# Optimization experiments

Measured on AMD Instinct MI355X. Metric: run time of the kernel, lower is better.

The kernel has to match this reference:

```python
import jax, jax.numpy as jnp
import numpy as np
import math

B, D, NH, HD, FF, P, IMG = 4, 768, 12, 64, 3072, 16, 256
L = (IMG // P) ** 2      # 256 tokens
PD = P * P * 3           # 768 patch dim
GRID = IMG // P          # 16


def setup_inputs() -> dict:
    key = jax.random.key(0)
    ks = iter(jax.random.split(key, 80))
    def nrm(shape, s=0.02):
        return jax.random.normal(next(ks), shape, jnp.float32) * s
    return {
        "x": jax.random.normal(next(ks), (B, 3, IMG, IMG), jnp.float32),
        "pe_norm_w": jnp.ones((PD,), jnp.float32),
        "pe_proj_w": nrm((PD, D)),
        "pe_proj_b": jnp.zeros((D,), jnp.float32),
        "pe_norm_out_w": jnp.ones((D,), jnp.float32),
        "pos_embed": nrm((1, L, D)),
        "in_attn_norm_w": jnp.ones((6, D), jnp.float32),
        "in_qkv_w": nrm((6, D, 3 * D)),
        "in_out_w": nrm((6, D, D)),
        "in_ff_norm_w": jnp.ones((6, D), jnp.float32),
        "in_w1": nrm((6, D, 2 * FF)),
        "in_w2": nrm((6, FF, D)),
        "mid_attn_norm_w": jnp.ones((3, D), jnp.float32),
        "mid_qkv_w": nrm((3, D, 3 * D)),
        "mid_out_w": nrm((3, D, D)),
        "mid_ff_norm_w": jnp.ones((3, D), jnp.float32),
        "mid_w1": nrm((3, D, 2 * FF)),
        "mid_w2": nrm((3, FF, D)),
        "out_skip_w": nrm((2 * D, D)),
        "out_skip_b": jnp.zeros((D,), jnp.float32),
        "out_attn_norm_w": jnp.ones((D,), jnp.float32),
        "out_qkv_w": nrm((D, 3 * D)),
        "out_out_w": nrm((D, D)),
        "out_ff_norm_w": jnp.ones((D,), jnp.float32),
        "out_w1": nrm((D, 2 * FF)),
        "out_w2": nrm((FF, D)),
        "final_norm_w": jnp.ones((D,), jnp.float32),
        "ol_proj_w": nrm((D, PD)),
        "ol_proj_b": jnp.zeros((PD,), jnp.float32),
        "rb_conv_in_w": nrm((128, 3, 3, 3), 0.1),
        "rb_gn_w": jnp.ones((5, 128), jnp.float32),
        "rb_gn_b": jnp.zeros((5, 128), jnp.float32),
        "rb_conv1_w": nrm((128, 1, 5, 5), 0.1),
        "rb_conv2_w": nrm((128, 1, 5, 5), 0.1),
        "head_conv_w": nrm((1, 128, 3, 3), 0.1),
    }


def _mish(x):
    return x * jnp.tanh(jax.nn.softplus(x))


def _rms(x, w, eps=1e-5):
    return x * jax.lax.rsqrt(jnp.mean(x * x, axis=-1, keepdims=True) + eps) * w


def _attn(x, qkv_w, out_w):
    b, l, _ = x.shape
    q, k, v = jnp.split(x @ qkv_w, 3, axis=-1)
    s = 1.0 / math.sqrt(HD)  # applied to BOTH q and k, as in source
    q = (q * s).reshape(b, l, NH, HD)
    k = (k * s).reshape(b, l, NH, HD)
    v = v.reshape(b, l, NH, HD)
    logits = jnp.einsum('bqhd,bkhd->bhqk', q, k).astype(jnp.float32)
    w = jax.nn.softmax(logits, axis=-1).astype(x.dtype)
    o = jnp.einsum('bhqk,bkhd->bqhd', w, v).reshape(b, l, NH * HD)
    return o @ out_w


def _ff(x, w1, w2):
    a, g = jnp.split(x @ w1, 2, axis=-1)
    return (_mish(a) * g) @ w2


def _block(x, an, qkv, ow, fn, w1, w2):
    x = x + _attn(_rms(x, an), qkv, ow)
    x = x + _ff(_rms(x, fn), w1, w2)
    return x


def _gn(x, w, b, groups=8, eps=1e-5):
    bb, c, h, ww = x.shape
    xg = x.reshape(bb, groups, c // groups, h, ww)
    m = jnp.mean(xg, axis=(2, 3, 4), keepdims=True)
    v = jnp.var(xg, axis=(2, 3, 4), keepdims=True)
    xn = ((xg - m) * jax.lax.rsqrt(v + eps)).reshape(bb, c, h, ww)
    return xn * w[:, None, None] + b[:, None, None]


def _conv(x, w, pad, dil=1, groups=1):
    xp = jnp.pad(x, ((0, 0), (0, 0), (pad, pad), (pad, pad)), mode='reflect')
    return jax.lax.conv_general_dilated(
        xp, w, window_strides=(1, 1), padding='VALID', rhs_dilation=(dil, dil),
        feature_group_count=groups, dimension_numbers=('NCHW', 'OIHW', 'NCHW'))


def _forward(x, pe_norm_w, pe_proj_w, pe_proj_b, pe_norm_out_w, pos_embed,
             in_attn_norm_w, in_qkv_w, in_out_w, in_ff_norm_w, in_w1, in_w2,
             mid_attn_norm_w, mid_qkv_w, mid_out_w, mid_ff_norm_w, mid_w1, mid_w2,
             out_skip_w, out_skip_b, out_attn_norm_w, out_qkv_w, out_out_w,
             out_ff_norm_w, out_w1, out_w2, final_norm_w, ol_proj_w, ol_proj_b,
             rb_conv_in_w, rb_gn_w, rb_gn_b, rb_conv1_w, rb_conv2_w, head_conv_w):
    b = x.shape[0]
    # PatchEmbed: b c (h p1) (w p2) -> b (h w) (p1 p2 c)
    t = x.reshape(b, 3, GRID, P, GRID, P).transpose(0, 2, 4, 3, 5, 1).reshape(b, L, PD)
    t = _rms(t, pe_norm_w)
    t = t @ pe_proj_w + pe_proj_b
    t = _rms(t, pe_norm_out_w)
    t = t + pos_embed
    # U-ViT trunk: 6 in blocks (skips saved), 3 middle, 1 out block (source typo -> single out block)
    skips = []
    for i in range(6):
        t = _block(t, in_attn_norm_w[i], in_qkv_w[i], in_out_w[i],
                   in_ff_norm_w[i], in_w1[i], in_w2[i])
        skips.append(t)
    for i in range(3):
        t = _block(t, mid_attn_norm_w[i], mid_qkv_w[i], mid_out_w[i],
                   mid_ff_norm_w[i], mid_w1[i], mid_w2[i])
    t = jnp.concatenate([t, skips[-1]], axis=-1) @ out_skip_w + out_skip_b
    t = _block(t, out_attn_norm_w, out_qkv_w, out_out_w, out_ff_norm_w, out_w1, out_w2)
    t = _rms(t, final_norm_w)
    # OutBlock: proj, dropout(eval=identity), unpatchify to b 3 256 256
    t = t @ ol_proj_w + ol_proj_b
    img = t.reshape(b, GRID, GRID, P, P, 3).transpose(0, 5, 1, 3, 2, 4).reshape(b, 3, IMG, IMG)
    # ResNetBlock(128)
    h = _conv(img, rb_conv_in_w, 1)
    h = _mish(_gn(h, rb_gn_w[0], rb_gn_b[0]))
    res = h
    h = _mish(_gn(_conv(h, rb_conv1_w, 2, 1, 128), rb_gn_w[1], rb_gn_b[1]))
    h = res + h
    h = _mish(_gn(h, rb_gn_w[2], rb_gn_b[2]))
    res = h
    h = _mish(_gn(_conv(h, rb_conv2_w, 6, 3, 128), rb_gn_w[3], rb_gn_b[3]))
    h = res + h
    h = _mish(_gn(h, rb_gn_w[4], rb_gn_b[4]))
    return _conv(h, head_conv_w, 1)  # [B, 1, 256, 256]


def reference(x, pe_norm_w, pe_proj_w, pe_proj_b, pe_norm_out_w, pos_embed,
              in_attn_norm_w, in_qkv_w, in_out_w, in_ff_norm_w, in_w1, in_w2,
              mid_attn_norm_w, mid_qkv_w, mid_out_w, mid_ff_norm_w, mid_w1, mid_w2,
              out_skip_w, out_skip_b, out_attn_norm_w, out_qkv_w, out_out_w,
              out_ff_norm_w, out_w1, out_w2, final_norm_w, ol_proj_w, ol_proj_b,
              rb_conv_in_w, rb_gn_w, rb_gn_b, rb_conv1_w, rb_conv2_w, head_conv_w):
    return _forward(x, pe_norm_w, pe_proj_w, pe_proj_b, pe_norm_out_w, pos_embed,
                    in_attn_norm_w, in_qkv_w, in_out_w, in_ff_norm_w, in_w1, in_w2,
                    mid_attn_norm_w, mid_qkv_w, mid_out_w, mid_ff_norm_w, mid_w1, mid_w2,
                    out_skip_w, out_skip_b, out_attn_norm_w, out_qkv_w, out_out_w,
                    out_ff_norm_w, out_w1, out_w2, final_norm_w, ol_proj_w, ol_proj_b,
                    rb_conv_in_w, rb_gn_w, rb_gn_b, rb_conv1_w, rb_conv2_w, head_conv_w)
```

## Files before the change

kernel.cpp:

```cpp
#include <hip/hip_runtime.h>
#include <math.h>

#define B_ 4
#define D_ 768
#define NH_ 12
#define HD_ 64
#define FF_ 3072
#define L_ 256
#define PD_ 768
#define GRID_ 16
#define P_ 16
#define IMG_ 256
#define M_ (B_*L_)
#define NCONV_ (B_*128*IMG_*IMG_)

typedef __attribute__((ext_vector_type(8))) short short8;
typedef __attribute__((ext_vector_type(4))) float f32x4;
typedef __attribute__((ext_vector_type(4))) unsigned short us4;
typedef __attribute__((ext_vector_type(8))) unsigned short us8;
typedef unsigned short ushort_t;

__device__ __forceinline__ float mishf(float x){
    float e = __expf(x);
    float u = (1.f + e) * (1.f + e);
    return x * (1.f - 2.f / (u + 1.f));
}

__device__ __forceinline__ int refl(int i, int n){
    if (i < 0) i = -i;
    if (i >= n) i = 2*n - 2 - i;
    return i;
}

__device__ __forceinline__ ushort_t f2bf(float f){
    unsigned int u = __float_as_uint(f);
    unsigned int r = (u + 0x7FFFu + ((u >> 16) & 1u)) >> 16;
    return (ushort_t)r;
}
__device__ __forceinline__ float bf2f(ushort_t u){
    return __uint_as_float(((unsigned int)u) << 16);
}

__device__ __forceinline__ void block_red2(float& s, float& q){
    #pragma unroll
    for (int o = 32; o > 0; o >>= 1){ s += __shfl_down(s, o); q += __shfl_down(q, o); }
    __shared__ float r1[4], r2[4];
    int tid = threadIdx.x;
    if ((tid & 63) == 0){ r1[tid>>6] = s; r2[tid>>6] = q; }
    __syncthreads();
    if (tid == 0){ s = r1[0]+r1[1]+r1[2]+r1[3]; q = r2[0]+r2[1]+r2[2]+r2[3]; }
    __syncthreads();
}

__global__ __launch_bounds__(256) void k_patchify(const float* __restrict__ x, float* __restrict__ t){
    int idx = blockIdx.x*256 + threadIdx.x;
    int d = idx % PD_; int l = (idx/PD_) % L_; int b = idx/(PD_*L_);
    int c = d % 3; int p = d / 3; int p1 = p / P_; int p2 = p % P_;
    int gh = l / GRID_; int gw = l % GRID_;
    int sy = gh*P_ + p1, sx = gw*P_ + p2;
    t[idx] = x[(((size_t)b*3 + c)*IMG_ + sy)*IMG_ + sx];
}

__global__ __launch_bounds__(256) void k_wt(const float* __restrict__ b0, const float* __restrict__ b1,
                                            const float* __restrict__ b2, int n0, int n1,
                                            ushort_t* __restrict__ dst, int K, int N){
    int z = blockIdx.z;
    size_t sz = (size_t)K * N;
    const float* src = (z < n0) ? b0 + (size_t)z*sz
                     : (z < n0+n1) ? b1 + (size_t)(z-n0)*sz
                     : b2 + (size_t)(z-n0-n1)*sz;
    ushort_t* out = dst + (size_t)z*sz;
    __shared__ float ld[32][33];
    int k0 = blockIdx.y*32, nc0 = blockIdx.x*32;
    int tid = threadIdx.x;
    int c = tid & 31, r8 = tid >> 5;
    #pragma unroll
    for (int i = 0; i < 4; ++i){
        int k = r8 + i*8;
        ld[k][c] = src[(size_t)(k0+k)*N + nc0 + c];
    }
    __syncthreads();
    #pragma unroll
    for (int i = 0; i < 4; ++i){
        int n = r8 + i*8;
        out[(size_t)(nc0+n)*K + k0 + c] = f2bf(ld[c][n]);
    }
}

template<bool OUT_BF>
__global__ __launch_bounds__(256) void k_rms(const float* __restrict__ x, const float* __restrict__ w,
                                             const float* __restrict__ addv, void* __restrict__ yv){
    int row = blockIdx.x;
    const float* xr = x + (size_t)row * D_;
    float s = 0.f;
    for (int i = threadIdx.x; i < D_; i += 256){ float v = xr[i]; s += v*v; }
    __shared__ float red[256];
    red[threadIdx.x] = s; __syncthreads();
    for (int o = 128; o > 0; o >>= 1){
        if (threadIdx.x < o) red[threadIdx.x] += red[threadIdx.x+o];
        __syncthreads();
    }
    float rstd = rsqrtf(red[0]/(float)D_ + 1e-5f);
    int l = row % L_;
    for (int i = threadIdx.x; i < D_; i += 256){
        float v = xr[i]*rstd*w[i];
        if (addv) v += addv[(size_t)l*D_ + i];
        if (OUT_BF) ((ushort_t*)yv)[(size_t)row*D_ + i] = f2bf(v);
        else        ((float*)yv)[(size_t)row*D_ + i] = v;
    }
}

template<bool OBF, int SPLITK>
__global__ __launch_bounds__(256) void k_gemm(const ushort_t* __restrict__ A, const ushort_t* __restrict__ Wt,
                                              void* __restrict__ Cv, const float* __restrict__ bias,
                                              const float* __restrict__ res, int N, int K){
    __shared__ ushort_t As[2][64][40];
    __shared__ ushort_t Ws[2][64][40];
    int tid = threadIdx.x;
    int lane = tid & 63, wid = tid >> 6;
    int wr = wid >> 1, wc = wid & 1;
    int row0 = blockIdx.y * 64, col0 = blockIdx.x * 64;
    f32x4 acc[2][2];
    #pragma unroll
    for (int i = 0; i < 2; ++i)
        #pragma unroll
        for (int j = 0; j < 2; ++j) acc[i][j] = (f32x4){0.f,0.f,0.f,0.f};

    int lg = lane >> 4, lr = lane & 15;
    int sr = tid >> 2, sk = (tid & 3) * 8;
    int kc = K / SPLITK;
    int k0 = (SPLITK > 1) ? blockIdx.z * kc : 0;
    const ushort_t* arow = A  + (size_t)(row0 + sr)*K + k0 + sk;
    const ushort_t* wrow = Wt + (size_t)(col0 + sr)*K + k0 + sk;

    for (int kt = 0; kt < kc; kt += 64){
        __syncthreads();
        *(short8*)&As[0][sr][sk] = *(const short8*)(arow + kt);
        *(short8*)&As[1][sr][sk] = *(const short8*)(arow + kt + 32);
        *(short8*)&Ws[0][sr][sk] = *(const short8*)(wrow + kt);
        *(short8*)&Ws[1][sr][sk] = *(const short8*)(wrow + kt + 32);
        __syncthreads();
        short8 a0[2], a1[2], b0[2], b1[2];
        #pragma unroll
        for (int i = 0; i < 2; ++i){
            a0[i] = *(const short8*)(&As[0][wr*32 + i*16 + lr][lg*8]);
            a1[i] = *(const short8*)(&As[1][wr*32 + i*16 + lr][lg*8]);
        }
        #pragma unroll
        for (int j = 0; j < 2; ++j){
            b0[j] = *(const short8*)(&Ws[0][wc*32 + j*16 + lr][lg*8]);
            b1[j] = *(const short8*)(&Ws[1][wc*32 + j*16 + lr][lg*8]);
        }
        #pragma unroll
        for (int i = 0; i < 2; ++i)
            #pragma unroll
            for (int j = 0; j < 2; ++j){
                acc[i][j] = __builtin_amdgcn_mfma_f32_16x16x32_bf16(a0[i], b0[j], acc[i][j], 0, 0, 0);
                acc[i][j] = __builtin_amdgcn_mfma_f32_16x16x32_bf16(a1[i], b1[j], acc[i][j], 0, 0, 0);
            }
    }
    if (SPLITK > 1){
        float* Pp = (float*)Cv + (size_t)blockIdx.z * M_ * N;
        #pragma unroll
        for (int i = 0; i < 2; ++i)
            #pragma unroll
            for (int j = 0; j < 2; ++j)
                #pragma unroll
                for (int q = 0; q < 4; ++q){
                    int m = row0 + wr*32 + i*16 + lg*4 + q;
                    int n = col0 + wc*32 + j*16 + lr;
                    Pp[(size_t)m*N + n] = acc[i][j][q];
                }
    } else {
        #pragma unroll
        for (int i = 0; i < 2; ++i)
            #pragma unroll
            for (int j = 0; j < 2; ++j)
                #pragma unroll
                for (int q = 0; q < 4; ++q){
                    int m = row0 + wr*32 + i*16 + lg*4 + q;
                    int n = col0 + wc*32 + j*16 + lr;
                    float v = acc[i][j][q];
                    if (bias) v += bias[n];
                    size_t o = (size_t)m*N + n;
                    if (OBF){
                        ((ushort_t*)Cv)[o] = f2bf(v);
                    } else {
                        if (res) v += res[o];
                        ((float*)Cv)[o] = v;
                    }
                }
    }
}

__global__ __launch_bounds__(256) void k_skred(const float* __restrict__ Pp, float* __restrict__ t){
    int idx = blockIdx.x*256 + threadIdx.x;
    size_t e = (size_t)idx*4;
    f32x4 s = *(const f32x4*)(t + e);
    #pragma unroll
    for (int z = 0; z < 4; ++z){
        f32x4 v = *(const f32x4*)(Pp + (size_t)z*M_*D_ + e);
        s.x += v.x; s.y += v.y; s.z += v.z; s.w += v.w;
    }
    *(f32x4*)(t + e) = s;
}

__global__ __launch_bounds__(256) void k_gemm_glu(const ushort_t* __restrict__ A, const ushort_t* __restrict__ Wt,
                                                  ushort_t* __restrict__ Cb, int K){
    __shared__ ushort_t As[2][64][40];
    __shared__ ushort_t Wa[2][64][40];
    __shared__ ushort_t Wg[2][64][40];
    int tid = threadIdx.x;
    int lane = tid & 63, wid = tid >> 6;
    int wr = wid >> 1, wc = wid & 1;
    int row0 = blockIdx.y * 64, col0 = blockIdx.x * 64;
    f32x4 aa[2][2], ag[2][2];
    #pragma unroll
    for (int i = 0; i < 2; ++i)
        #pragma unroll
        for (int j = 0; j < 2; ++j){ aa[i][j] = (f32x4){0.f,0.f,0.f,0.f}; ag[i][j] = (f32x4){0.f,0.f,0.f,0.f}; }

    int lg = lane >> 4, lr = lane & 15;
    int sr = tid >> 2, sk = (tid & 3) * 8;
    const ushort_t* arow = A + (size_t)(row0+sr)*K + sk;
    const ushort_t* war = Wt + (size_t)(col0+sr)*K + sk;
    const ushort_t* wgr = Wt + (size_t)(FF_+col0+sr)*K + sk;

    for (int kt = 0; kt < K; kt += 64){
        __syncthreads();
        *(short8*)&As[0][sr][sk] = *(const short8*)(arow + kt);
        *(short8*)&As[1][sr][sk] = *(const short8*)(arow + kt + 32);
        *(short8*)&Wa[0][sr][sk] = *(const short8*)(war + kt);
        *(short8*)&Wa[1][sr][sk] = *(const short8*)(war + kt + 32);
        *(short8*)&Wg[0][sr][sk] = *(const short8*)(wgr + kt);
        *(short8*)&Wg[1][sr][sk] = *(const short8*)(wgr + kt + 32);
        __syncthreads();
        short8 a0[2], a1[2], ba0[2], ba1[2], bg0[2], bg1[2];
        #pragma unroll
        for (int i = 0; i < 2; ++i){
            a0[i] = *(const short8*)(&As[0][wr*32 + i*16 + lr][lg*8]);
            a1[i] = *(const short8*)(&As[1][wr*32 + i*16 + lr][lg*8]);
        }
        #pragma unroll
        for (int j = 0; j < 2; ++j){
            ba0[j] = *(const short8*)(&Wa[0][wc*32 + j*16 + lr][lg*8]);
            ba1[j] = *(const short8*)(&Wa[1][wc*32 + j*16 + lr][lg*8]);
            bg0[j] = *(const short8*)(&Wg[0][wc*32 + j*16 + lr][lg*8]);
            bg1[j] = *(const short8*)(&Wg[1][wc*32 + j*16 + lr][lg*8]);
        }
        #pragma unroll
        for (int i = 0; i < 2; ++i)
            #pragma unroll
            for (int j = 0; j < 2; ++j){
                aa[i][j] = __builtin_amdgcn_mfma_f32_16x16x32_bf16(a0[i], ba0[j], aa[i][j], 0, 0, 0);
                aa[i][j] = __builtin_amdgcn_mfma_f32_16x16x32_bf16(a1[i], ba1[j], aa[i][j], 0, 0, 0);
                ag[i][j] = __builtin_amdgcn_mfma_f32_16x16x32_bf16(a0[i], bg0[j], ag[i][j], 0, 0, 0);
                ag[i][j] = __builtin_amdgcn_mfma_f32_16x16x32_bf16(a1[i], bg1[j], ag[i][j], 0, 0, 0);
            }
    }
    #pragma unroll
    for (int i = 0; i < 2; ++i)
        #pragma unroll
        for (int j = 0; j < 2; ++j)
            #pragma unroll
            for (int q = 0; q < 4; ++q){
                int m = row0 + wr*32 + i*16 + lg*4 + q;
                int n = col0 + wc*32 + j*16 + lr;
                Cb[(size_t)m*FF_ + n] = f2bf(mishf(aa[i][j][q]) * ag[i][j][q]);
            }
}

__global__ __launch_bounds__(256) void k_attn(const ushort_t* __restrict__ qkv, ushort_t* __restrict__ out){
    int qt = blockIdx.x, h = blockIdx.y, b = blockIdx.z;
    const ushort_t* base = qkv + (size_t)b * L_ * 3 * D_;
    __shared__ ushort_t Qs[64][72];
    __shared__ ushort_t KVs[64][72];
    __shared__ ushort_t Ps[64][268];
    __shared__ float red[8][64];
    int tid = threadIdx.x;
    int lane = tid & 63, w = tid >> 6;
    int lr = lane & 15, lg = lane >> 4;

    {
        int r = tid >> 2, c = (tid & 3) * 16;
        const ushort_t* src = base + (size_t)(qt*64 + r)*3*D_ + h*HD_ + c;
        *(us8*)&Qs[r][c]   = *(const us8*)src;
        *(us8*)&Qs[r][c+8] = *(const us8*)(src + 8);
    }

    f32x4 sacc[4][4];
    #pragma unroll
    for (int kt = 0; kt < 4; ++kt)
        #pragma unroll
        for (int mi = 0; mi < 4; ++mi) sacc[kt][mi] = (f32x4){0.f,0.f,0.f,0.f};

    for (int kt = 0; kt < 4; ++kt){
        __syncthreads();
        {
            int r = tid >> 2, c = (tid & 3) * 16;
            const ushort_t* src = base + (size_t)(kt*64 + r)*3*D_ + D_ + h*HD_ + c;
            *(us8*)&KVs[r][c]   = *(const us8*)src;
            *(us8*)&KVs[r][c+8] = *(const us8*)(src + 8);
        }
        __syncthreads();
        short8 bk0 = *(const short8*)&KVs[w*16 + lr][lg*8];
        short8 bk1 = *(const short8*)&KVs[w*16 + lr][32 + lg*8];
        #pragma unroll
        for (int mi = 0; mi < 4; ++mi){
            short8 a0 = *(const short8*)&Qs[mi*16 + lr][lg*8];
            short8 a1 = *(const short8*)&Qs[mi*16 + lr][32 + lg*8];
            sacc[kt][mi] = __builtin_amdgcn_mfma_f32_16x16x32_bf16(a0, bk0, sacc[kt][mi], 0, 0, 0);
            sacc[kt][mi] = __builtin_amdgcn_mfma_f32_16x16x32_bf16(a1, bk1, sacc[kt][mi], 0, 0, 0);
        }
    }

    const float inv64 = 1.0f/64.0f;
    float gm[4][4], linv[4][4];
    #pragma unroll
    for (int mi = 0; mi < 4; ++mi){
        #pragma unroll
        for (int r = 0; r < 4; ++r){
            float v = fmaxf(fmaxf(sacc[0][mi][r], sacc[1][mi][r]), fmaxf(sacc[2][mi][r], sacc[3][mi][r]));
            v = fmaxf(v, __shfl_xor(v, 1));
            v = fmaxf(v, __shfl_xor(v, 2));
            v = fmaxf(v, __shfl_xor(v, 4));
            v = fmaxf(v, __shfl_xor(v, 8));
            gm[mi][r] = v;
            if (lr == 0) red[w][mi*16 + lg*4 + r] = v;
        }
    }
    __syncthreads();
    #pragma unroll
    for (int mi = 0; mi < 4; ++mi){
        #pragma unroll
        for (int r = 0; r < 4; ++r){
            int row = mi*16 + lg*4 + r;
            float m = fmaxf(fmaxf(red[0][row], red[1][row]), fmaxf(red[2][row], red[3][row]));
            gm[mi][r] = m;
            float sum = 0.f;
            #pragma unroll
            for (int kt = 0; kt < 4; ++kt){
                float p = __expf((sacc[kt][mi][r] - m) * inv64);
                Ps[row][kt*64 + w*16 + lr] = f2bf(p);
                sum += p;
            }
            sum += __shfl_xor(sum, 1);
            sum += __shfl_xor(sum, 2);
            sum += __shfl_xor(sum, 4);
            sum += __shfl_xor(sum, 8);
            linv[mi][r] = sum;
            if (lr == 0) red[4 + w][row] = sum;
        }
    }
    __syncthreads();
    #pragma unroll
    for (int mi = 0; mi < 4; ++mi){
        #pragma unroll
        for (int r = 0; r < 4; ++r){
            int row = mi*16 + lg*4 + r;
            linv[mi][r] = 1.0f / (red[4][row] + red[5][row] + red[6][row] + red[7][row]);
        }
    }

    f32x4 oacc[4];
    #pragma unroll
    for (int mi = 0; mi < 4; ++mi) oacc[mi] = (f32x4){0.f,0.f,0.f,0.f};
    for (int kt = 0; kt < 4; ++kt){
        __syncthreads();
        {
            int k = tid & 63, dg = tid >> 6;
            const ushort_t* src = base + (size_t)(kt*64 + k)*3*D_ + 2*D_ + h*HD_ + dg*16;
            us8 v0 = *(const us8*)src;
            us8 v1 = *(const us8*)(src + 8);
            #pragma unroll
            for (int j = 0; j < 8; ++j) KVs[dg*16 + j][k] = v0[j];
            #pragma unroll
            for (int j = 0; j < 8; ++j) KVs[dg*16 + 8 + j][k] = v1[j];
        }
        __syncthreads();
        short8 bv0 = *(const short8*)&KVs[w*16 + lr][lg*8];
        short8 bv1 = *(const short8*)&KVs[w*16 + lr][32 + lg*8];
        #pragma unroll
        for (int mi = 0; mi < 4; ++mi){
            short8 a0 = *(const short8*)&Ps[mi*16 + lr][kt*64 + lg*8];
            short8 a1 = *(const short8*)&Ps[mi*16 + lr][kt*64 + 32 + lg*8];
            oacc[mi] = __builtin_amdgcn_mfma_f32_16x16x32_bf16(a0, bv0, oacc[mi], 0, 0, 0);
            oacc[mi] = __builtin_amdgcn_mfma_f32_16x16x32_bf16(a1, bv1, oacc[mi], 0, 0, 0);
        }
    }
    #pragma unroll
    for (int mi = 0; mi < 4; ++mi){
        #pragma unroll
        for (int r = 0; r < 4; ++r){
            int row = mi*16 + lg*4 + r;
            out[((size_t)(b*L_ + qt*64 + row))*D_ + h*HD_ + w*16 + lr] = f2bf(oacc[mi][r] * linv[mi][r]);
        }
    }
}

__global__ __launch_bounds__(256) void k_cat(const float* __restrict__ t, const float* __restrict__ skip,
                                             ushort_t* __restrict__ cat){
    int i4 = (blockIdx.x*256 + threadIdx.x) * 4;
    int r = i4 / D_, c = i4 % D_;
    float4 a = *(const float4*)(t + i4);
    float4 b = *(const float4*)(skip + i4);
    us4 ua, ub;
    ua.x=f2bf(a.x); ua.y=f2bf(a.y); ua.z=f2bf(a.z); ua.w=f2bf(a.w);
    ub.x=f2bf(b.x); ub.y=f2bf(b.y); ub.z=f2bf(b.z); ub.w=f2bf(b.w);
    *(us4*)(cat + (size_t)r*1536 + c) = ua;
    *(us4*)(cat + (size_t)r*1536 + 768 + c) = ub;
}

__global__ __launch_bounds__(256) void k_unpatchify(const float* __restrict__ t, float* __restrict__ img){
    int idx = blockIdx.x*256 + threadIdx.x;
    int sx = idx % IMG_; int sy = (idx/IMG_)%IMG_; int c = (idx/(IMG_*IMG_))%3; int b = idx/(3*IMG_*IMG_);
    int gh = sy / P_, p1 = sy % P_, gw = sx / P_, p2 = sx % P_;
    img[idx] = t[(((size_t)b*L_) + gh*GRID_+gw)*PD_ + (p1*P_+p2)*3 + c];
}

__global__ __launch_bounds__(256) void k_conv_in(const float* __restrict__ img, const float* __restrict__ w,
                                                 ushort_t* __restrict__ out, float* __restrict__ partial){
    int y = blockIdx.x, b = blockIdx.y;
    int x = threadIdx.x;
    __shared__ float rows[9][IMG_];
    int yy0 = refl(y-1, IMG_), yy2 = refl(y+1, IMG_);
    #pragma unroll
    for (int ic = 0; ic < 3; ++ic){
        const float* basep = img + ((size_t)(b*3+ic))*IMG_*IMG_;
        rows[ic*3+0][x] = basep[(size_t)yy0*IMG_ + x];
        rows[ic*3+1][x] = basep[(size_t)y  *IMG_ + x];
        rows[ic*3+2][x] = basep[(size_t)yy2*IMG_ + x];
    }
    __syncthreads();
    int xl = (x==0)?1:x-1, xr = (x==255)?254:x+1;
    float sg = 0.f, qg = 0.f;
    for (int oc = 0; oc < 128; ++oc){
        const float* wv = w + oc*27;
        float acc = 0.f;
        #pragma unroll
        for (int ic = 0; ic < 3; ++ic){
            const float* wk = wv + ic*9;
            acc += rows[ic*3+0][xl]*wk[0] + rows[ic*3+0][x]*wk[1] + rows[ic*3+0][xr]*wk[2]
                 + rows[ic*3+1][xl]*wk[3] + rows[ic*3+1][x]*wk[4] + rows[ic*3+1][xr]*wk[5]
                 + rows[ic*3+2][xl]*wk[6] + rows[ic*3+2][x]*wk[7] + rows[ic*3+2][xr]*wk[8];
        }
        out[(((size_t)(b*128+oc))*IMG_ + y)*IMG_ + x] = f2bf(acc);
        sg += acc; qg += acc*acc;
        if ((oc & 15) == 15){
            block_red2(sg, qg);
            if (threadIdx.x == 0){
                int pidx = ((b*8 + (oc>>4))*256 + y);
                partial[pidx*2] = sg; partial[pidx*2+1] = qg;
            }
            sg = 0.f; qg = 0.f;
        }
    }
}

__global__ __launch_bounds__(256) void k_gn_fin(const float* __restrict__ partial, int nper,
                                                float* __restrict__ stats){
    int bg = blockIdx.x, tid = threadIdx.x;
    float s = 0.f, q = 0.f;
    for (int i = tid; i < nper; i += 256){
        s += partial[((size_t)bg*nper + i)*2];
        q += partial[((size_t)bg*nper + i)*2 + 1];
    }
    block_red2(s, q);
    if (tid == 0){
        const float n = 16.f*IMG_*IMG_;
        float m = s/n;
        float var = q/n - m*m;
        stats[bg*2]   = m;
        stats[bg*2+1] = rsqrtf(var + 1e-5f);
    }
}

__global__ __launch_bounds__(256) void k_act(const ushort_t* __restrict__ x, const float* __restrict__ st,
                                             const float* __restrict__ gw, const float* __restrict__ gb,
                                             ushort_t* __restrict__ y){
    int bid = blockIdx.x;
    int b = bid >> 11, c = (bid >> 4) & 127;
    int bg = b*8 + (c>>4);
    float sc = st[bg*2+1]*gw[c], sb = gb[c] - st[bg*2]*sc;
    size_t e0 = (size_t)bid*4096 + threadIdx.x*16;
    us8 v0 = *(const us8*)(x + e0), v1 = *(const us8*)(x + e0 + 8);
    us8 r0, r1;
    #pragma unroll
    for (int i = 0; i < 8; ++i) r0[i] = f2bf(mishf(bf2f(v0[i])*sc + sb));
    #pragma unroll
    for (int i = 0; i < 8; ++i) r1[i] = f2bf(mishf(bf2f(v1[i])*sc + sb));
    *(us8*)(y + e0) = r0;
    *(us8*)(y + e0 + 8) = r1;
}

template<int PAD, int DIL>
__global__ __launch_bounds__(256) void k_dw(const ushort_t* __restrict__ in,
                                            const float* __restrict__ cw,
                                            ushort_t* __restrict__ out, float* __restrict__ partial){
    constexpr int S = 32 + 2*PAD;
    constexpr int SP = (DIL == 1) ? 40 : 52;
    __shared__ float tile[S*SP];
    int tileid = blockIdx.x, c = blockIdx.y, b = blockIdx.z;
    int x0 = (tileid & 7) * 32, y0 = (tileid >> 3) * 32;
    int tid = threadIdx.x;
    const ushort_t* ip = in + ((size_t)(b*128+c))*IMG_*IMG_;
    for (int i = tid; i < S*S; i += 256){
        int r = i / S, cc = i - r*S;
        int gy = refl(y0 - PAD + r, IMG_);
        int gx = refl(x0 - PAD + cc, IMG_);
        tile[r*SP + cc] = bf2f(ip[(size_t)gy*IMG_ + gx]);
    }
    __syncthreads();
    const float* wc = cw + c*25;
    int tx4 = (tid & 7) * 4, ty = tid >> 3;
    float acc[4] = {0.f,0.f,0.f,0.f};
    constexpr int NW = 4*DIL + 4;
    #pragma unroll
    for (int kh = 0; kh < 5; ++kh){
        const float* rowp = &tile[(ty + kh*DIL)*SP + tx4];
        float vv[NW];
        #pragma unroll
        for (int qq = 0; qq < NW/4; ++qq){
            f32x4 v = *(const f32x4*)(rowp + qq*4);
            vv[qq*4+0]=v.x; vv[qq*4+1]=v.y; vv[qq*4+2]=v.z; vv[qq*4+3]=v.w;
        }
        #pragma unroll
        for (int kw = 0; kw < 5; ++kw){
            float wk = wc[kh*5+kw];
            #pragma unroll
            for (int j = 0; j < 4; ++j)
                acc[j] += vv[kw*DIL + j] * wk;
        }
    }
    us4 o4;
    o4.x = f2bf(acc[0]); o4.y = f2bf(acc[1]); o4.z = f2bf(acc[2]); o4.w = f2bf(acc[3]);
    *(us4*)(out + (((size_t)(b*128+c))*IMG_ + y0+ty)*IMG_ + x0+tx4) = o4;
    float s = acc[0]+acc[1]+acc[2]+acc[3];
    float q = acc[0]*acc[0]+acc[1]*acc[1]+acc[2]*acc[2]+acc[3]*acc[3];
    block_red2(s, q);
    if (tid == 0){
        int bid = (b*128 + c)*64 + tileid;
        partial[bid*2] = s; partial[bid*2+1] = q;
    }
}

__global__ __launch_bounds__(256) void k_addmish(const ushort_t* __restrict__ xn, const float* __restrict__ stn,
                                                 const float* __restrict__ wn, const float* __restrict__ bn,
                                                 const ushort_t* __restrict__ resa,
                                                 ushort_t* __restrict__ out, float* __restrict__ partial){
    int bid = blockIdx.x;
    int b = bid >> 11, c = (bid >> 4) & 127;
    int bg = b*8 + (c>>4);
    float scn = stn[bg*2+1]*wn[c], sbn = bn[c] - stn[bg*2]*scn;
    size_t e0 = (size_t)bid*4096 + threadIdx.x*16;
    us8 vn0 = *(const us8*)(xn + e0), vn1 = *(const us8*)(xn + e0 + 8);
    us8 vr0 = *(const us8*)(resa + e0), vr1 = *(const us8*)(resa + e0 + 8);
    us8 r0, r1;
    float s = 0.f, q = 0.f;
    #pragma unroll
    for (int i = 0; i < 8; ++i){
        float v = mishf(bf2f(vn0[i])*scn + sbn) + bf2f(vr0[i]);
        s += v; q += v*v; r0[i] = f2bf(v);
    }
    #pragma unroll
    for (int i = 0; i < 8; ++i){
        float v = mishf(bf2f(vn1[i])*scn + sbn) + bf2f(vr1[i]);
        s += v; q += v*v; r1[i] = f2bf(v);
    }
    *(us8*)(out + e0) = r0;
    *(us8*)(out + e0 + 8) = r1;
    block_red2(s, q);
    if (threadIdx.x == 0){ partial[bid*2] = s; partial[bid*2+1] = q; }
}

__global__ __launch_bounds__(256) void k_head_part(const ushort_t* __restrict__ in, const float* __restrict__ st,
                                                   const float* __restrict__ gw, const float* __restrict__ gb,
                                                   const float* __restrict__ w, float* __restrict__ part){
    __shared__ float tile[34*34];
    int tileid = blockIdx.x, cg = blockIdx.y, b = blockIdx.z;
    int x0 = (tileid & 7)*32, y0 = (tileid >> 3)*32;
    int tid = threadIdx.x;
    int tx4 = (tid & 7)*4, ty = tid >> 3;
    float m  = st[(b*8+cg)*2];
    float rs = st[(b*8+cg)*2 + 1];
    float acc[4] = {0.f,0.f,0.f,0.f};
    for (int ci = 0; ci < 16; ++ci){
        int c = cg*16 + ci;
        float sc = rs*gw[c], sb = gb[c] - m*sc;
        const ushort_t* ip = in + ((size_t)(b*128+c))*IMG_*IMG_;
        if (ci) __syncthreads();
        for (int i = tid; i < 34*34; i += 256){
            int r = i/34, cc = i - r*34;
            int gy = refl(y0-1+r, IMG_);
            int gx = refl(x0-1+cc, IMG_);
            tile[i] = mishf(bf2f(ip[(size_t)gy*IMG_+gx])*sc + sb);
        }
        __syncthreads();
        const float* wc = w + c*9;
        #pragma unroll
        for (int kh = 0; kh < 3; ++kh){
            float vv[6];
            #pragma unroll
            for (int u = 0; u < 6; ++u) vv[u] = tile[(ty+kh)*34 + tx4 + u];
            #pragma unroll
            for (int kw = 0; kw < 3; ++kw){
                float wk = wc[kh*3+kw];
                #pragma unroll
                for (int j = 0; j < 4; ++j) acc[j] += vv[kw+j]*wk;
            }
        }
    }
    f32x4 o = {acc[0], acc[1], acc[2], acc[3]};
    *(f32x4*)(part + (((size_t)(cg*4+b))*IMG_ + y0+ty)*IMG_ + x0+tx4) = o;
}

__global__ __launch_bounds__(256) void k_head_fin(const float* __restrict__ part, float* __restrict__ out){
    int idx4 = blockIdx.x*256 + threadIdx.x;
    size_t e = (size_t)idx4*4;
    int b = (int)(e / (IMG_*IMG_));
    size_t off = e % (IMG_*IMG_);
    f32x4 s = {0.f,0.f,0.f,0.f};
    #pragma unroll
    for (int cg = 0; cg < 8; ++cg){
        f32x4 v = *(const f32x4*)(part + (size_t)(cg*4+b)*IMG_*IMG_ + off);
        s.x += v.x; s.y += v.y; s.z += v.z; s.w += v.w;
    }
    *(f32x4*)(out + e) = s;
}


struct WsMap {
    float *t, *skip, *t2, *ybuf, *img, *partial, *hpart, *stats, *part;
    ushort_t *nb, *qkvb, *ab, *gbuf, *cat, *wb_qkv, *wb_out, *wb_w1, *wb_w2, *wb_pe, *wb_skip, *wb_ol, *cA, *cB;
};

static void run_block(const float* an, const ushort_t* qw, const ushort_t* ow,
                      const float* fn, const ushort_t* w1, const ushort_t* w2,
                      float* t, const WsMap& W, hipStream_t stream){
    k_rms<true><<<M_, 256, 0, stream>>>(t, an, nullptr, W.nb);
    k_gemm<true,1><<<dim3(3*D_/64, M_/64), 256, 0, stream>>>(W.nb, qw, W.qkvb, nullptr, nullptr, 3*D_, D_);
    k_attn<<<dim3(4, NH_, B_), 256, 0, stream>>>(W.qkvb, W.ab);
    k_gemm<false,1><<<dim3(D_/64, M_/64), 256, 0, stream>>>(W.ab, ow, t, nullptr, t, D_, D_);
    k_rms<true><<<M_, 256, 0, stream>>>(t, fn, nullptr, W.nb);
    k_gemm_glu<<<dim3(FF_/64, M_/64), 256, 0, stream>>>(W.nb, w1, W.gbuf, D_);
    k_gemm<false,4><<<dim3(D_/64, M_/64, 4), 256, 0, stream>>>(W.gbuf, w2, W.part, nullptr, nullptr, D_, FF_);
    k_skred<<<(M_*D_)/1024, 256, 0, stream>>>(W.part, t);
}

extern "C" void kernel_launch(void* const* d_in, const int* in_sizes, int n_in,
                              void* d_out, int out_size, void* d_ws, size_t ws_size,
                              hipStream_t stream){
    const float* x              = (const float*)d_in[0];
    const float* pe_norm_w      = (const float*)d_in[1];
    const float* pe_proj_w      = (const float*)d_in[2];
    const float* pe_proj_b      = (const float*)d_in[3];
    const float* pe_norm_out_w  = (const float*)d_in[4];
    const float* pos_embed      = (const float*)d_in[5];
    const float* in_attn_norm_w = (const float*)d_in[6];
    const float* in_qkv_w       = (const float*)d_in[7];
    const float* in_out_w       = (const float*)d_in[8];
    const float* in_ff_norm_w   = (const float*)d_in[9];
    const float* in_w1          = (const float*)d_in[10];
    const float* in_w2          = (const float*)d_in[11];
    const float* mid_attn_norm_w= (const float*)d_in[12];
    const float* mid_qkv_w      = (const float*)d_in[13];
    const float* mid_out_w      = (const float*)d_in[14];
    const float* mid_ff_norm_w  = (const float*)d_in[15];
    const float* mid_w1         = (const float*)d_in[16];
    const float* mid_w2         = (const float*)d_in[17];
    const float* out_skip_w     = (const float*)d_in[18];
    const float* out_skip_b     = (const float*)d_in[19];
    const float* out_attn_norm_w= (const float*)d_in[20];
    const float* out_qkv_w      = (const float*)d_in[21];
    const float* out_out_w      = (const float*)d_in[22];
    const float* out_ff_norm_w  = (const float*)d_in[23];
    const float* out_w1         = (const float*)d_in[24];
    const float* out_w2         = (const float*)d_in[25];
    const float* final_norm_w   = (const float*)d_in[26];
    const float* ol_proj_w      = (const float*)d_in[27];
    const float* ol_proj_b      = (const float*)d_in[28];
    const float* rb_conv_in_w   = (const float*)d_in[29];
    const float* rb_gn_w        = (const float*)d_in[30];
    const float* rb_gn_b        = (const float*)d_in[31];
    const float* rb_conv1_w     = (const float*)d_in[32];
    const float* rb_conv2_w     = (const float*)d_in[33];
    const float* head_conv_w    = (const float*)d_in[34];

    WsMap W;
    float* f = (float*)d_ws;
    const size_t TD = (size_t)M_*D_;
    W.t      = f;               f += TD;
    W.skip   = f;               f += TD;
    W.t2     = f;               f += TD;
    W.ybuf   = f;               f += TD;
    W.img    = f;               f += TD;
    W.partial= f;               f += 131072;
    W.hpart  = f;               f += (size_t)8*4*IMG_*IMG_;
    W.stats  = f;               f += 448;
    W.part   = f;               f += (size_t)4*TD;
    ushort_t* u = (ushort_t*)f;
    W.nb     = u;               u += TD;
    W.qkvb   = u;               u += (size_t)M_*3*D_;
    W.ab     = u;               u += TD;
    W.gbuf   = u;               u += (size_t)M_*FF_;
    W.cat    = u;               u += (size_t)M_*2*D_;
    W.wb_qkv = u;               u += (size_t)10*D_*3*D_;
    W.wb_out = u;               u += (size_t)10*D_*D_;
    W.wb_w1  = u;               u += (size_t)10*D_*2*FF_;
    W.wb_w2  = u;               u += (size_t)10*FF_*D_;
    W.wb_pe  = u;               u += (size_t)D_*D_;
    W.wb_skip= u;               u += (size_t)2*D_*D_;
    W.wb_ol  = u;               u += (size_t)D_*D_;
    W.cA     = u;               u += (size_t)NCONV_;
    W.cB     = u;

    float* st0 = W.stats;       float* st1 = W.stats + 64;
    float* st2 = W.stats + 128; float* st3 = W.stats + 192;
    float* st4 = W.stats + 256;

    k_wt<<<dim3(3*D_/32, D_/32, 10), 256, 0, stream>>>(in_qkv_w, mid_qkv_w, out_qkv_w, 6, 3, W.wb_qkv, D_, 3*D_);
    k_wt<<<dim3(D_/32, D_/32, 10), 256, 0, stream>>>(in_out_w, mid_out_w, out_out_w, 6, 3, W.wb_out, D_, D_);
    k_wt<<<dim3(2*FF_/32, D_/32, 10), 256, 0, stream>>>(in_w1, mid_w1, out_w1, 6, 3, W.wb_w1, D_, 2*FF_);
    k_wt<<<dim3(D_/32, FF_/32, 10), 256, 0, stream>>>(in_w2, mid_w2, out_w2, 6, 3, W.wb_w2, FF_, D_);
    k_wt<<<dim3(D_/32, D_/32, 1), 256, 0, stream>>>(pe_proj_w, nullptr, nullptr, 1, 0, W.wb_pe, D_, D_);
    k_wt<<<dim3(D_/32, 2*D_/32, 1), 256, 0, stream>>>(out_skip_w, nullptr, nullptr, 1, 0, W.wb_skip, 2*D_, D_);
    k_wt<<<dim3(D_/32, D_/32, 1), 256, 0, stream>>>(ol_proj_w, nullptr, nullptr, 1, 0, W.wb_ol, D_, D_);

    k_patchify<<<(B_*L_*PD_)/256, 256, 0, stream>>>(x, W.t2);
    k_rms<true><<<M_, 256, 0, stream>>>(W.t2, pe_norm_w, nullptr, W.nb);
    k_gemm<false,1><<<dim3(D_/64, M_/64), 256, 0, stream>>>(W.nb, W.wb_pe, W.t, pe_proj_b, nullptr, D_, D_);
    k_rms<false><<<M_, 256, 0, stream>>>(W.t, pe_norm_out_w, pos_embed, W.t);

    for (int i = 0; i < 6; ++i){
        run_block(in_attn_norm_w + (size_t)i*D_, W.wb_qkv + (size_t)i*D_*3*D_,
                  W.wb_out + (size_t)i*D_*D_, in_ff_norm_w + (size_t)i*D_,
                  W.wb_w1 + (size_t)i*D_*2*FF_, W.wb_w2 + (size_t)i*FF_*D_,
                  W.t, W, stream);
    }
    hipMemcpyAsync(W.skip, W.t, TD*sizeof(float), hipMemcpyDeviceToDevice, stream);

    for (int i = 0; i < 3; ++i){
        int z = 6 + i;
        run_block(mid_attn_norm_w + (size_t)i*D_, W.wb_qkv + (size_t)z*D_*3*D_,
                  W.wb_out + (size_t)z*D_*D_, mid_ff_norm_w + (size_t)i*D_,
                  W.wb_w1 + (size_t)z*D_*2*FF_, W.wb_w2 + (size_t)z*FF_*D_,
                  W.t, W, stream);
    }

    k_cat<<<(M_*D_)/1024, 256, 0, stream>>>(W.t, W.skip, W.cat);
    k_gemm<false,1><<<dim3(D_/64, M_/64), 256, 0, stream>>>(W.cat, W.wb_skip, W.t2, out_skip_b, nullptr, D_, 2*D_);

    run_block(out_attn_norm_w, W.wb_qkv + (size_t)9*D_*3*D_, W.wb_out + (size_t)9*D_*D_,
              out_ff_norm_w, W.wb_w1 + (size_t)9*D_*2*FF_, W.wb_w2 + (size_t)9*FF_*D_,
              W.t2, W, stream);

    k_rms<true><<<M_, 256, 0, stream>>>(W.t2, final_norm_w, nullptr, W.nb);
    k_gemm<false,1><<<dim3(PD_/64, M_/64), 256, 0, stream>>>(W.nb, W.wb_ol, W.ybuf, ol_proj_b, nullptr, PD_, D_);
    k_unpatchify<<<(B_*3*IMG_*IMG_)/256, 256, 0, stream>>>(W.ybuf, W.img);

    k_conv_in<<<dim3(256, 4), 256, 0, stream>>>(W.img, rb_conv_in_w, W.cA, W.partial);
    k_gn_fin<<<32, 256, 0, stream>>>(W.partial, 256, st0);
    k_act<<<8192, 256, 0, stream>>>(W.cA, st0, rb_gn_w, rb_gn_b, W.cB);
    k_dw<2,1><<<dim3(64, 128, 4), 256, 0, stream>>>(W.cB, rb_conv1_w, W.cA, W.partial);
    k_gn_fin<<<32, 256, 0, stream>>>(W.partial, 1024, st1);
    k_addmish<<<8192, 256, 0, stream>>>(W.cA, st1, rb_gn_w+128, rb_gn_b+128, W.cB, W.cA, W.partial);
    k_gn_fin<<<32, 256, 0, stream>>>(W.partial, 256, st2);
    k_act<<<8192, 256, 0, stream>>>(W.cA, st2, rb_gn_w+256, rb_gn_b+256, W.cB);
    k_dw<6,3><<<dim3(64, 128, 4), 256, 0, stream>>>(W.cB, rb_conv2_w, W.cA, W.partial);
    k_gn_fin<<<32, 256, 0, stream>>>(W.partial, 1024, st3);
    k_addmish<<<8192, 256, 0, stream>>>(W.cA, st3, rb_gn_w+384, rb_gn_b+384, W.cB, W.cA, W.partial);
    k_gn_fin<<<32, 256, 0, stream>>>(W.partial, 256, st4);
    k_head_part<<<dim3(64, 8, 4), 256, 0, stream>>>(W.cA, st4, rb_gn_w+512, rb_gn_b+512, head_conv_w, W.hpart);
    k_head_fin<<<(B_*IMG_*IMG_)/1024, 256, 0, stream>>>(W.hpart, (float*)d_out);
}
```

Measured before the change: 1.550 ms.

## Enlarge depthwise conv tiles, vectorize halo loads, keep weights in registers

The depthwise 5x5 conv kernels now compute 32x64 output tiles per block instead of 32x32, with each thread producing two rows. This halves the block count and the halo overhead per output. Interior tiles load the input with aligned 4-wide vector reads, using a padded column offset. The 25 filter weights are hoisted into registers, and the GroupNorm partial count is adjusted to match the new grid. The cost is more shared memory and registers per block, plus fewer blocks available to hide latency.

```diff
diff --git a/kernel.cpp b/kernel.cpp
--- a/kernel.cpp
+++ b/kernel.cpp
@@ -497,50 +497,69 @@
 __global__ __launch_bounds__(256) void k_dw(const ushort_t* __restrict__ in,
                                             const float* __restrict__ cw,
                                             ushort_t* __restrict__ out, float* __restrict__ partial){
-    constexpr int S = 32 + 2*PAD;
-    constexpr int SP = (DIL == 1) ? 40 : 52;
-    __shared__ float tile[S*SP];
+    constexpr int AP = (DIL==1) ? 4 : 8;
+    constexpr int SC = (DIL==1) ? 44 : 52;
+    constexpr int SY = 64 + 2*PAD;
+    constexpr int CH = SC/4;
+    __shared__ float tile[SY*SC];
     int tileid = blockIdx.x, c = blockIdx.y, b = blockIdx.z;
-    int x0 = (tileid & 7) * 32, y0 = (tileid >> 3) * 32;
+    int x0 = (tileid & 7) * 32, y0 = (tileid >> 3) * 64;
     int tid = threadIdx.x;
     const ushort_t* ip = in + ((size_t)(b*128+c))*IMG_*IMG_;
-    for (int i = tid; i < S*S; i += 256){
-        int r = i / S, cc = i - r*S;
-        int gy = refl(y0 - PAD + r, IMG_);
-        int gx = refl(x0 - PAD + cc, IMG_);
-        tile[r*SP + cc] = bf2f(ip[(size_t)gy*IMG_ + gx]);
+    int xs = x0 - AP;
+    if (xs >= 0 && xs + SC <= IMG_){
+        for (int j = tid; j < SY*CH; j += 256){
+            int r = j / CH, q = j - r*CH;
+            int gy = refl(y0 - PAD + r, IMG_);
+            us4 v = *(const us4*)(ip + (size_t)gy*IMG_ + xs + q*4);
+            f32x4 fv = { bf2f(v.x), bf2f(v.y), bf2f(v.z), bf2f(v.w) };
+            *(f32x4*)&tile[r*SC + q*4] = fv;
+        }
+    } else {
+        for (int j = tid; j < SY*SC; j += 256){
+            int r = j / SC, cc = j - r*SC;
+            int gy = refl(y0 - PAD + r, IMG_);
+            int gx = refl(xs + cc, IMG_);
+            tile[r*SC + cc] = bf2f(ip[(size_t)gy*IMG_ + gx]);
+        }
     }
     __syncthreads();
-    const float* wc = cw + c*25;
-    int tx4 = (tid & 7) * 4, ty = tid >> 3;
-    float acc[4] = {0.f,0.f,0.f,0.f};
-    constexpr int NW = 4*DIL + 4;
-    #pragma unroll
-    for (int kh = 0; kh < 5; ++kh){
-        const float* rowp = &tile[(ty + kh*DIL)*SP + tx4];
-        float vv[NW];
-        #pragma unroll
-        for (int qq = 0; qq < NW/4; ++qq){
-            f32x4 v = *(const f32x4*)(rowp + qq*4);
-            vv[qq*4+0]=v.x; vv[qq*4+1]=v.y; vv[qq*4+2]=v.z; vv[qq*4+3]=v.w;
-        }
-        #pragma unroll
-        for (int kw = 0; kw < 5; ++kw){
-            float wk = wc[kh*5+kw];
-            #pragma unroll
-            for (int j = 0; j < 4; ++j)
-                acc[j] += vv[kw*DIL + j] * wk;
-        }
-    }
-    us4 o4;
-    o4.x = f2bf(acc[0]); o4.y = f2bf(acc[1]); o4.z = f2bf(acc[2]); o4.w = f2bf(acc[3]);
-    *(us4*)(out + (((size_t)(b*128+c))*IMG_ + y0+ty)*IMG_ + x0+tx4) = o4;
-    float s = acc[0]+acc[1]+acc[2]+acc[3];
-    float q = acc[0]*acc[0]+acc[1]*acc[1]+acc[2]*acc[2]+acc[3]*acc[3];
-    block_red2(s, q);
+    float wreg[25];
+    #pragma unroll
+    for (int u = 0; u < 25; ++u) wreg[u] = cw[c*25 + u];
+    int tx4 = (tid & 7)*4, ty = tid >> 3;
+    constexpr int NV = (DIL==1) ? 3 : 5;
+    float s = 0.f, q2 = 0.f;
+    #pragma unroll
+    for (int rr = 0; rr < 2; ++rr){
+        int yy = ty + rr*32;
+        float acc[4] = {0.f,0.f,0.f,0.f};
+        #pragma unroll
+        for (int kh = 0; kh < 5; ++kh){
+            const float* rowp = &tile[(yy + kh*DIL)*SC + tx4];
+            float vv[NV*4];
+            #pragma unroll
+            for (int u = 0; u < NV; ++u){
+                f32x4 v = *(const f32x4*)(rowp + u*4);
+                vv[u*4]=v.x; vv[u*4+1]=v.y; vv[u*4+2]=v.z; vv[u*4+3]=v.w;
+            }
+            #pragma unroll
+            for (int kw = 0; kw < 5; ++kw){
+                float wk = wreg[kh*5+kw];
+                #pragma unroll
+                for (int j = 0; j < 4; ++j)
+                    acc[j] += vv[kw*DIL + j + (AP - 2*DIL)] * wk;
+            }
+        }
+        us4 o4 = { f2bf(acc[0]), f2bf(acc[1]), f2bf(acc[2]), f2bf(acc[3]) };
+        *(us4*)(out + (((size_t)(b*128+c))*IMG_ + y0+yy)*IMG_ + x0+tx4) = o4;
+        s  += acc[0]+acc[1]+acc[2]+acc[3];
+        q2 += acc[0]*acc[0]+acc[1]*acc[1]+acc[2]*acc[2]+acc[3]*acc[3];
+    }
+    block_red2(s, q2);
     if (tid == 0){
-        int bid = (b*128 + c)*64 + tileid;
-        partial[bid*2] = s; partial[bid*2+1] = q;
+        int bid = (b*128 + c)*32 + tileid;
+        partial[bid*2] = s; partial[bid*2+1] = q2;
     }
 }
 
@@ -761,13 +780,13 @@
     k_conv_in<<<dim3(256, 4), 256, 0, stream>>>(W.img, rb_conv_in_w, W.cA, W.partial);
     k_gn_fin<<<32, 256, 0, stream>>>(W.partial, 256, st0);
     k_act<<<8192, 256, 0, stream>>>(W.cA, st0, rb_gn_w, rb_gn_b, W.cB);
-    k_dw<2,1><<<dim3(64, 128, 4), 256, 0, stream>>>(W.cB, rb_conv1_w, W.cA, W.partial);
-    k_gn_fin<<<32, 256, 0, stream>>>(W.partial, 1024, st1);
+    k_dw<2,1><<<dim3(32, 128, 4), 256, 0, stream>>>(W.cB, rb_conv1_w, W.cA, W.partial);
+    k_gn_fin<<<32, 256, 0, stream>>>(W.partial, 512, st1);
     k_addmish<<<8192, 256, 0, stream>>>(W.cA, st1, rb_gn_w+128, rb_gn_b+128, W.cB, W.cA, W.partial);
     k_gn_fin<<<32, 256, 0, stream>>>(W.partial, 256, st2);
     k_act<<<8192, 256, 0, stream>>>(W.cA, st2, rb_gn_w+256, rb_gn_b+256, W.cB);
-    k_dw<6,3><<<dim3(64, 128, 4), 256, 0, stream>>>(W.cB, rb_conv2_w, W.cA, W.partial);
-    k_gn_fin<<<32, 256, 0, stream>>>(W.partial, 1024, st3);
+    k_dw<6,3><<<dim3(32, 128, 4), 256, 0, stream>>>(W.cB, rb_conv2_w, W.cA, W.partial);
+    k_gn_fin<<<32, 256, 0, stream>>>(W.partial, 512, st3);
     k_addmish<<<8192, 256, 0, stream>>>(W.cA, st3, rb_gn_w+384, rb_gn_b+384, W.cB, W.cA, W.partial);
     k_gn_fin<<<32, 256, 0, stream>>>(W.partial, 256, st4);
     k_head_part<<<dim3(64, 8, 4), 256, 0, stream>>>(W.cA, st4, rb_gn_w+512, rb_gn_b+512, head_conv_w, W.hpart);
```

Result: no change. 1.533 ms (-1.1%).
